# Optimization experiments

Measured on AMD Instinct MI355X. Metric: run time of the kernel, lower is better.

## Reference

```python
import jax, jax.numpy as jnp
import numpy as np
import math

B, C, H, W = 16, 256, 128, 128
N = 4096
D = 256  # out_channels
IMG = 512


def _bilinear_sample(features, grid):
    """features (B,C,H,W), grid (B,N,2) in [-1,1] (x,y). align_corners=True, border padding."""
    Bq, Cq, Hq, Wq = features.shape
    ix = (grid[..., 0] + 1.0) * 0.5 * (Wq - 1)  # (B,N)
    iy = (grid[..., 1] + 1.0) * 0.5 * (Hq - 1)
    # border padding: clamp continuous coords into valid range
    ix = jnp.clip(ix, 0.0, Wq - 1)
    iy = jnp.clip(iy, 0.0, Hq - 1)
    x0 = jnp.floor(ix)
    y0 = jnp.floor(iy)
    wx = ix - x0
    wy = iy - y0
    x0i = jnp.clip(x0.astype(jnp.int32), 0, Wq - 1)
    y0i = jnp.clip(y0.astype(jnp.int32), 0, Hq - 1)
    x1i = jnp.clip(x0i + 1, 0, Wq - 1)
    y1i = jnp.clip(y0i + 1, 0, Hq - 1)
    f = features.reshape(Bq, Cq, Hq * Wq)

    def gather(yi, xi):
        idx = (yi * Wq + xi)[:, None, :]  # (B,1,N)
        return jnp.take_along_axis(f, idx, axis=2)  # (B,C,N)

    v00 = gather(y0i, x0i)
    v01 = gather(y0i, x1i)
    v10 = gather(y1i, x0i)
    v11 = gather(y1i, x1i)
    wx = wx[:, None, :]
    wy = wy[:, None, :]
    top = v00 * (1 - wx) + v01 * wx
    bot = v10 * (1 - wx) + v11 * wx
    return top * (1 - wy) + bot * wy  # (B,C,N)


def _pos_encoding(positions, d_model):
    """positions (B,N,2) in [0,1] -> (B,N,2*d_model) sinusoidal."""
    div_term = jnp.exp(jnp.arange(0, d_model, 2, dtype=jnp.float32)
                       * (-math.log(10000.0) / d_model))  # (d_model//2,)
    x = positions[..., 0:1] * 1000.0  # (B,N,1)
    y = positions[..., 1:2] * 1000.0

    def interleave(v):
        a = v * div_term  # (B,N,d_model//2)
        sc = jnp.stack([jnp.sin(a), jnp.cos(a)], axis=-1)  # (B,N,d//2,2)
        return sc.reshape(*v.shape[:-1], d_model)

    return jnp.concatenate([interleave(x), interleave(y)], axis=-1)


def setup_inputs() -> dict:
    key = jax.random.key(0)
    ks = jax.random.split(key, 8)
    features = jax.random.normal(ks[0], (B, C, H, W), dtype=jnp.float32)
    vertices = jax.random.uniform(ks[1], (B, N, 2), dtype=jnp.float32) * IMG
    s1 = 1.0 / math.sqrt(C)
    s2 = 1.0 / math.sqrt(D)
    W1 = jax.random.uniform(ks[2], (C, D), jnp.float32, -s1, s1)
    b1 = jnp.zeros((D,), jnp.float32)
    W2 = jax.random.uniform(ks[3], (D, D), jnp.float32, -s2, s2)
    b2 = jnp.zeros((D,), jnp.float32)
    Wp = jax.random.uniform(ks[4], (D, D), jnp.float32, -s2, s2)
    bp = jnp.zeros((D,), jnp.float32)
    return {"features": features, "vertices": vertices, "image_size": IMG,
            "W1": W1, "b1": b1, "W2": W2, "b2": b2, "Wp": Wp, "bp": bp}


def reference(features, vertices, image_size, W1, b1, W2, b2, Wp, bp):
    # normalize pixel coords to [-1,1] (align_corners=True convention)
    denom = jnp.float32(image_size - 1)
    grid = 2.0 * vertices / denom - 1.0  # (B,N,2)
    sampled = _bilinear_sample(features, grid)  # (B,C,N)
    sampled = jnp.transpose(sampled, (0, 2, 1))  # (B,N,C)
    h = jax.nn.relu(jnp.einsum('bnc,cd->bnd', sampled, W1) + b1)
    vfeat = jnp.einsum('bnd,de->bne', h, W2) + b2  # (B,N,D)
    pos_enc = _pos_encoding(vertices / jnp.float32(image_size), D // 2)  # (B,N,D)
    out = jnp.einsum('bnd,de->bne', vfeat + pos_enc, Wp) + bp
    return out
```

## Files before the change

### kernel.cpp

```cpp
#include <hip/hip_runtime.h>

#define HW 16384
#define Nn 4096

typedef __bf16 bf16x8 __attribute__((ext_vector_type(8)));
typedef unsigned short us8t __attribute__((ext_vector_type(8)));
typedef float f32x4 __attribute__((ext_vector_type(4)));
typedef float f32x16 __attribute__((ext_vector_type(16)));

__device__ __forceinline__ unsigned short f2bf(float f) {
    unsigned int u = __float_as_uint(f);
    u = (u + 0x7fffu + ((u >> 16) & 1u)) >> 16;
    return (unsigned short)u;
}
__device__ __forceinline__ float bf2f(unsigned int h) {
    return __uint_as_float(h << 16);
}
__device__ __forceinline__ f32x4 mfma16(us8t a, us8t b, f32x4 c) {
    return __builtin_amdgcn_mfma_f32_16x16x32_bf16(
        __builtin_bit_cast(bf16x8, a), __builtin_bit_cast(bf16x8, b), c, 0, 0, 0);
}
__device__ __forceinline__ f32x16 mfma32(us8t a, us8t b, f32x16 c) {
    return __builtin_amdgcn_mfma_f32_32x32x16_bf16(
        __builtin_bit_cast(bf16x8, a), __builtin_bit_cast(bf16x8, b), c, 0, 0, 0);
}

__global__ __launch_bounds__(256) void k_wt(const float* __restrict__ W1,
                                            const float* __restrict__ W2,
                                            const float* __restrict__ Wp,
                                            unsigned short* __restrict__ WT) {
    const int m = blockIdx.x >> 8;
    const int d = blockIdx.x & 255;
    const int c = threadIdx.x;
    const float* W = (m == 0) ? W1 : (m == 1) ? W2 : Wp;
    WT[m * 65536 + d * 256 + c] = f2bf(W[c * 256 + d]);
}

__global__ __launch_bounds__(256) void k_gemm1(const float* __restrict__ f,
                                               const unsigned short* __restrict__ W1T,
                                               unsigned short* __restrict__ S, int b0) {
    __shared__ __align__(16) unsigned short Asb[2][64][32];

    int blk = blockIdx.x;
    if ((gridDim.x & 7) == 0) {
        const int chunk = gridDim.x >> 3;
        blk = (blk & 7) * chunk + (blk >> 3);
    }
    const int bl = blk >> 8;
    const int b = b0 + bl;
    const int p0 = (blk & 255) << 6;
    const int t = threadIdx.x;
    const int lane = t & 63;
    const int w = t >> 6;
    const int l5 = lane >> 5;
    const int r31 = lane & 31;

    const float* fb = f + ((size_t)b << 22) + p0 + lane;

    unsigned short* wP = &Asb[0][lane][(w ^ ((lane >> 2) & 3)) << 3];
    const int G = (r31 >> 2) & 3;
    const unsigned short* rP0 = &Asb[0][r31][(l5 ^ G) << 3];
    const unsigned short* rP1 = &Asb[0][r31][((2 + l5) ^ G) << 3];

    f32x16 acc[2][2];
#pragma unroll
    for (int i = 0; i < 2; ++i)
#pragma unroll
        for (int j = 0; j < 2; ++j)
#pragma unroll
            for (int r = 0; r < 16; ++r) acc[i][j][r] = 0.f;

    const unsigned short* Bp0 = W1T + (((w << 6) + r31) << 8) + (l5 << 3);
    const unsigned short* Bp1 = Bp0 + (32 << 8);

    float pf[8];
#pragma unroll
    for (int j = 0; j < 8; ++j) pf[j] = fb[(size_t)((w << 3) + j) << 14];

    us8t bnx[2][2];
    bnx[0][0] = *(const us8t*)(Bp0);
    bnx[0][1] = *(const us8t*)(Bp0 + 16);
    bnx[1][0] = *(const us8t*)(Bp1);
    bnx[1][1] = *(const us8t*)(Bp1 + 16);

    for (int k0 = 0; k0 < 256; k0 += 32) {
        const int bo = ((k0 >> 5) & 1) << 11;

        uint4 pk;
        pk.x = (unsigned)f2bf(pf[0]) | ((unsigned)f2bf(pf[1]) << 16);
        pk.y = (unsigned)f2bf(pf[2]) | ((unsigned)f2bf(pf[3]) << 16);
        pk.z = (unsigned)f2bf(pf[4]) | ((unsigned)f2bf(pf[5]) << 16);
        pk.w = (unsigned)f2bf(pf[6]) | ((unsigned)f2bf(pf[7]) << 16);
        *(uint4*)(wP + bo) = pk;

        us8t bcur[2][2];
        bcur[0][0] = bnx[0][0]; bcur[0][1] = bnx[0][1];
        bcur[1][0] = bnx[1][0]; bcur[1][1] = bnx[1][1];

        if (k0 < 224) {
#pragma unroll
            for (int j = 0; j < 8; ++j)
                pf[j] = fb[(size_t)(k0 + 32 + (w << 3) + j) << 14];
            bnx[0][0] = *(const us8t*)(Bp0 + k0 + 32);
            bnx[0][1] = *(const us8t*)(Bp0 + k0 + 48);
            bnx[1][0] = *(const us8t*)(Bp1 + k0 + 32);
            bnx[1][1] = *(const us8t*)(Bp1 + k0 + 48);
        }

        __syncthreads();

        us8t af[2][2];
        af[0][0] = *(const us8t*)(rP0 + bo);
        af[0][1] = *(const us8t*)(rP1 + bo);
        af[1][0] = *(const us8t*)(rP0 + bo + 1024);
        af[1][1] = *(const us8t*)(rP1 + bo + 1024);

#pragma unroll
        for (int mt = 0; mt < 2; ++mt)
#pragma unroll
            for (int nt = 0; nt < 2; ++nt) {
                acc[mt][nt] = mfma32(af[mt][0], bcur[nt][0], acc[mt][nt]);
                acc[mt][nt] = mfma32(af[mt][1], bcur[nt][1], acc[mt][nt]);
            }
    }

    unsigned short* Sp = S + ((((size_t)bl << 14) + p0) << 8);
    const int rbase = l5 << 2;
#pragma unroll
    for (int mt = 0; mt < 2; ++mt)
#pragma unroll
        for (int nt = 0; nt < 2; ++nt) {
            const int d = (w << 6) + (nt << 5) + r31;
#pragma unroll
            for (int r = 0; r < 16; ++r) {
                const int row = (mt << 5) + ((r >> 2) << 3) + (r & 3) + rbase;
                Sp[((size_t)row << 8) + d] = f2bf(acc[mt][nt][r]);
            }
        }
}

__global__ __launch_bounds__(256) void k_fused(const unsigned short* __restrict__ S,
                                               const float* __restrict__ verts,
                                               const int* __restrict__ iszp,
                                               const unsigned short* __restrict__ W2T,
                                               const unsigned short* __restrict__ WpT,
                                               const float* __restrict__ b1,
                                               const float* __restrict__ b2,
                                               const float* __restrict__ bpv,
                                               float* __restrict__ out, int b0) {
    __shared__ __align__(16) unsigned short hT[64][264];
    __shared__ __align__(16) int pIdx[64][4];
    __shared__ __align__(16) float wBl[64][4];
    __shared__ float vps[64][2];
    __shared__ __align__(16) float b1s[256];
    __shared__ float b2s[256], bps[256];

    const int blk = blockIdx.x;
    const int bl = blk >> 6;
    const int b = b0 + bl;
    const int n0 = (blk & 63) << 6;
    const int t = threadIdx.x;
    const int lane = t & 63;
    const int w = t >> 6;

    b1s[t] = b1[t];
    b2s[t] = b2[t];
    bps[t] = bpv[t];

    if (t < 64) {
        const float isz = (float)iszp[0];
        const size_t vo = ((size_t)b * Nn + n0 + t) << 1;
        const float vx = verts[vo + 0];
        const float vy = verts[vo + 1];
        const float gs = 127.0f / (isz - 1.0f);
        const float ix = fminf(fmaxf(vx * gs, 0.0f), 127.0f);
        const float iy = fminf(fmaxf(vy * gs, 0.0f), 127.0f);
        const float x0 = floorf(ix), y0 = floorf(iy);
        const float wx = ix - x0, wy = iy - y0;
        const int x0i = (int)x0, y0i = (int)y0;
        const int x1i = min(x0i + 1, 127), y1i = min(y0i + 1, 127);
        pIdx[t][0] = (y0i << 7) + x0i;
        pIdx[t][1] = (y0i << 7) + x1i;
        pIdx[t][2] = (y1i << 7) + x0i;
        pIdx[t][3] = (y1i << 7) + x1i;
        wBl[t][0] = (1.0f - wx) * (1.0f - wy);
        wBl[t][1] = wx * (1.0f - wy);
        wBl[t][2] = (1.0f - wx) * wy;
        wBl[t][3] = wx * wy;
        vps[t][0] = vx / isz;
        vps[t][1] = vy / isz;
    }
    __syncthreads();

    {
        const unsigned short* Sb = S + ((size_t)bl << 22);
        const float4 bl1 = *(const float4*)&b1s[lane << 2];
        for (int i = 0; i < 16; ++i) {
            const int r = (w << 4) + i;
            const int4 pp = *(const int4*)pIdx[r];
            const float4 wt = *(const float4*)wBl[r];
            const uint2 a0 = *(const uint2*)(Sb + ((size_t)pp.x << 8) + (lane << 2));
            const uint2 a1 = *(const uint2*)(Sb + ((size_t)pp.y << 8) + (lane << 2));
            const uint2 a2 = *(const uint2*)(Sb + ((size_t)pp.z << 8) + (lane << 2));
            const uint2 a3 = *(const uint2*)(Sb + ((size_t)pp.w << 8) + (lane << 2));
            float d0 = wt.x * bf2f(a0.x & 0xffffu) + wt.y * bf2f(a1.x & 0xffffu) +
                       wt.z * bf2f(a2.x & 0xffffu) + wt.w * bf2f(a3.x & 0xffffu) + bl1.x;
            float d1 = wt.x * bf2f(a0.x >> 16) + wt.y * bf2f(a1.x >> 16) +
                       wt.z * bf2f(a2.x >> 16) + wt.w * bf2f(a3.x >> 16) + bl1.y;
            float d2 = wt.x * bf2f(a0.y & 0xffffu) + wt.y * bf2f(a1.y & 0xffffu) +
                       wt.z * bf2f(a2.y & 0xffffu) + wt.w * bf2f(a3.y & 0xffffu) + bl1.z;
            float d3 = wt.x * bf2f(a0.y >> 16) + wt.y * bf2f(a1.y >> 16) +
                       wt.z * bf2f(a2.y >> 16) + wt.w * bf2f(a3.y >> 16) + bl1.w;
            d0 = fmaxf(d0, 0.0f);
            d1 = fmaxf(d1, 0.0f);
            d2 = fmaxf(d2, 0.0f);
            d3 = fmaxf(d3, 0.0f);
            uint2 pk;
            pk.x = (unsigned)f2bf(d0) | ((unsigned)f2bf(d1) << 16);
            pk.y = (unsigned)f2bf(d2) | ((unsigned)f2bf(d3) << 16);
            *(uint2*)&hT[r][lane << 2] = pk;
        }
    }
    __syncthreads();

    const int mrow = lane & 15;
    const int kg = (lane >> 4) << 3;
    const int r0 = (lane >> 4) << 2;
    const int n0w = w << 6;

    f32x4 acc[4][4];
#pragma unroll
    for (int i = 0; i < 4; ++i)
#pragma unroll
        for (int j = 0; j < 4; ++j) acc[i][j] = (f32x4){0.f, 0.f, 0.f, 0.f};

    us8t bnx[4];
#pragma unroll
    for (int nt = 0; nt < 4; ++nt)
        bnx[nt] = *(const us8t*)(W2T + ((n0w + (nt << 4) + mrow) << 8) + kg);
    for (int k0 = 0; k0 < 256; k0 += 32) {
        us8t bcur[4];
#pragma unroll
        for (int nt = 0; nt < 4; ++nt) bcur[nt] = bnx[nt];
        if (k0 < 224) {
#pragma unroll
            for (int nt = 0; nt < 4; ++nt)
                bnx[nt] = *(const us8t*)(W2T + ((n0w + (nt << 4) + mrow) << 8) + k0 + 32 + kg);
        }
        us8t af[4];
#pragma unroll
        for (int mt = 0; mt < 4; ++mt)
            af[mt] = *(const us8t*)&hT[(mt << 4) + mrow][k0 + kg];
#pragma unroll
        for (int mt = 0; mt < 4; ++mt)
#pragma unroll
            for (int nt = 0; nt < 4; ++nt)
                acc[mt][nt] = mfma16(af[mt], bcur[nt], acc[mt][nt]);
    }
    __syncthreads();

    const float C2 = -0.20762050593046f;
#pragma unroll
    for (int nt = 0; nt < 4; ++nt) {
        const int col = n0w + (nt << 4) + mrow;
        const float bias2 = b2s[col];
        const int ci = col & 127;
        const float dv = exp2f((float)(ci >> 1) * C2) * 1000.0f;
        const int sel = col >> 7;
#pragma unroll
        for (int mt = 0; mt < 4; ++mt)
#pragma unroll
            for (int j = 0; j < 4; ++j) {
                const int row = (mt << 4) + r0 + j;
                const float ang = vps[row][sel] * dv;
                const float pe = (col & 1) ? __cosf(ang) : __sinf(ang);
                hT[row][col] = f2bf(acc[mt][nt][j] + bias2 + pe);
            }
    }
    __syncthreads();

#pragma unroll
    for (int i = 0; i < 4; ++i)
#pragma unroll
        for (int j = 0; j < 4; ++j) acc[i][j] = (f32x4){0.f, 0.f, 0.f, 0.f};
#pragma unroll
    for (int nt = 0; nt < 4; ++nt)
        bnx[nt] = *(const us8t*)(WpT + ((n0w + (nt << 4) + mrow) << 8) + kg);
    for (int k0 = 0; k0 < 256; k0 += 32) {
        us8t bcur[4];
#pragma unroll
        for (int nt = 0; nt < 4; ++nt) bcur[nt] = bnx[nt];
        if (k0 < 224) {
#pragma unroll
            for (int nt = 0; nt < 4; ++nt)
                bnx[nt] = *(const us8t*)(WpT + ((n0w + (nt << 4) + mrow) << 8) + k0 + 32 + kg);
        }
        us8t af[4];
#pragma unroll
        for (int mt = 0; mt < 4; ++mt)
            af[mt] = *(const us8t*)&hT[(mt << 4) + mrow][k0 + kg];
#pragma unroll
        for (int mt = 0; mt < 4; ++mt)
#pragma unroll
            for (int nt = 0; nt < 4; ++nt)
                acc[mt][nt] = mfma16(af[mt], bcur[nt], acc[mt][nt]);
    }

    float* ob = out + (((size_t)b * Nn + n0) << 8);
#pragma unroll
    for (int nt = 0; nt < 4; ++nt) {
        const int col = n0w + (nt << 4) + mrow;
        const float bb = bps[col];
#pragma unroll
        for (int mt = 0; mt < 4; ++mt)
#pragma unroll
            for (int j = 0; j < 4; ++j) {
                const int row = (mt << 4) + r0 + j;
                ob[((size_t)row << 8) + col] = acc[mt][nt][j] + bb;
            }
    }
}

extern "C" void kernel_launch(void* const* d_in, const int* in_sizes, int n_in,
                              void* d_out, int out_size, void* d_ws, size_t ws_size,
                              hipStream_t stream) {
    const float* f = (const float*)d_in[0];
    const float* verts = (const float*)d_in[1];
    const int* isz = (const int*)d_in[2];
    const float* W1 = (const float*)d_in[3];
    const float* b1 = (const float*)d_in[4];
    const float* W2 = (const float*)d_in[5];
    const float* b2 = (const float*)d_in[6];
    const float* Wp = (const float*)d_in[7];
    const float* bp = (const float*)d_in[8];
    float* out = (float*)d_out;

    unsigned short* WT = (unsigned short*)d_ws;
    const size_t S_OFF = 512u << 10;
    unsigned short* S = (unsigned short*)((char*)d_ws + S_OFF);

    const size_t perBatch = (size_t)HW * 256 * 2;
    size_t sbytes = (ws_size > S_OFF) ? (ws_size - S_OFF) : 0;
    int nbMax = (int)(sbytes / perBatch);
    if (nbMax < 1) nbMax = 1;
    if (nbMax > 16) nbMax = 16;

    k_wt<<<dim3(768), dim3(256), 0, stream>>>(W1, W2, Wp, WT);
    for (int b0 = 0; b0 < 16; b0 += nbMax) {
        const int nb = (16 - b0 < nbMax) ? (16 - b0) : nbMax;
        k_gemm1<<<dim3(nb * 256), dim3(256), 0, stream>>>(f, WT, S, b0);
        k_fused<<<dim3(nb * 64), dim3(256), 0, stream>>>(S, verts, isz, WT + 65536, WT + 131072,
                                                         b1, b2, bp, out, b0);
    }
}
```

Measured before the change: 525.4 us.

## Restructure first GEMM with larger tiles and async global-to-LDS fp32 staging

The feature-projection GEMM is rebuilt around 512-thread blocks, each covering 256 pixels by all 256 output channels instead of 64 pixels. Feature tiles of 64 channels are copied as fp32 straight from global memory into double-buffered shared memory with the global_load_lds builtin, and converted to bf16 when read for MFMA. W1T fragments are now loaded from global memory inside the inner loop instead of being prefetched into registers. The aim is to cut register round-trips and grid count, and to overlap the feature stream with compute. The cost is 128 KB of LDS per block, which limits residency to one block per CU despite the launch bound of two, plus repeated conversions on every LDS read.

```diff
diff --git a/kernel.cpp b/kernel.cpp
--- a/kernel.cpp
+++ b/kernel.cpp
@@ -23,6 +23,12 @@
 __device__ __forceinline__ f32x16 mfma32(us8t a, us8t b, f32x16 c) {
     return __builtin_amdgcn_mfma_f32_32x32x16_bf16(
         __builtin_bit_cast(bf16x8, a), __builtin_bit_cast(bf16x8, b), c, 0, 0, 0);
+}
+
+__device__ __forceinline__ void gload16(const float* g, float* l) {
+    __builtin_amdgcn_global_load_lds(
+        (const __attribute__((address_space(1))) unsigned int*)g,
+        (__attribute__((address_space(3))) unsigned int*)l, 16, 0, 0);
 }
 
 __global__ __launch_bounds__(256) void k_wt(const float* __restrict__ W1,
@@ -36,92 +42,76 @@
     WT[m * 65536 + d * 256 + c] = f2bf(W[c * 256 + d]);
 }
 
-__global__ __launch_bounds__(256) void k_gemm1(const float* __restrict__ f,
-                                               const unsigned short* __restrict__ W1T,
-                                               unsigned short* __restrict__ S, int b0) {
-    __shared__ __align__(16) unsigned short Asb[2][64][32];
+__global__ __launch_bounds__(512, 2) void k_gemm1(const float* __restrict__ f,
+                                                  const unsigned short* __restrict__ W1T,
+                                                  unsigned short* __restrict__ S, int b0) {
+    __shared__ __align__(16) float fs[2][64][256];
 
     int blk = blockIdx.x;
     if ((gridDim.x & 7) == 0) {
         const int chunk = gridDim.x >> 3;
         blk = (blk & 7) * chunk + (blk >> 3);
     }
-    const int bl = blk >> 8;
+    const int bl = blk >> 6;
     const int b = b0 + bl;
-    const int p0 = (blk & 255) << 6;
+    const int p0 = (blk & 63) << 8;
     const int t = threadIdx.x;
     const int lane = t & 63;
     const int w = t >> 6;
     const int l5 = lane >> 5;
     const int r31 = lane & 31;
-
-    const float* fb = f + ((size_t)b << 22) + p0 + lane;
-
-    unsigned short* wP = &Asb[0][lane][(w ^ ((lane >> 2) & 3)) << 3];
-    const int G = (r31 >> 2) & 3;
-    const unsigned short* rP0 = &Asb[0][r31][(l5 ^ G) << 3];
-    const unsigned short* rP1 = &Asb[0][r31][((2 + l5) ^ G) << 3];
-
-    f32x16 acc[2][2];
+    const int wp = w & 3;
+    const int wd = w >> 2;
+
+    const float* fb = f + ((size_t)b << 22) + p0;
+
+    f32x16 acc[2][4];
 #pragma unroll
     for (int i = 0; i < 2; ++i)
 #pragma unroll
-        for (int j = 0; j < 2; ++j)
+        for (int j = 0; j < 4; ++j)
 #pragma unroll
             for (int r = 0; r < 16; ++r) acc[i][j][r] = 0.f;
 
-    const unsigned short* Bp0 = W1T + (((w << 6) + r31) << 8) + (l5 << 3);
-    const unsigned short* Bp1 = Bp0 + (32 << 8);
-
-    float pf[8];
-#pragma unroll
-    for (int j = 0; j < 8; ++j) pf[j] = fb[(size_t)((w << 3) + j) << 14];
-
-    us8t bnx[2][2];
-    bnx[0][0] = *(const us8t*)(Bp0);
-    bnx[0][1] = *(const us8t*)(Bp0 + 16);
-    bnx[1][0] = *(const us8t*)(Bp1);
-    bnx[1][1] = *(const us8t*)(Bp1 + 16);
-
-    for (int k0 = 0; k0 < 256; k0 += 32) {
-        const int bo = ((k0 >> 5) & 1) << 11;
-
-        uint4 pk;
-        pk.x = (unsigned)f2bf(pf[0]) | ((unsigned)f2bf(pf[1]) << 16);
-        pk.y = (unsigned)f2bf(pf[2]) | ((unsigned)f2bf(pf[3]) << 16);
-        pk.z = (unsigned)f2bf(pf[4]) | ((unsigned)f2bf(pf[5]) << 16);
-        pk.w = (unsigned)f2bf(pf[6]) | ((unsigned)f2bf(pf[7]) << 16);
-        *(uint4*)(wP + bo) = pk;
-
-        us8t bcur[2][2];
-        bcur[0][0] = bnx[0][0]; bcur[0][1] = bnx[0][1];
-        bcur[1][0] = bnx[1][0]; bcur[1][1] = bnx[1][1];
-
-        if (k0 < 224) {
-#pragma unroll
-            for (int j = 0; j < 8; ++j)
-                pf[j] = fb[(size_t)(k0 + 32 + (w << 3) + j) << 14];
-            bnx[0][0] = *(const us8t*)(Bp0 + k0 + 32);
-            bnx[0][1] = *(const us8t*)(Bp0 + k0 + 48);
-            bnx[1][0] = *(const us8t*)(Bp1 + k0 + 32);
-            bnx[1][1] = *(const us8t*)(Bp1 + k0 + 48);
-        }
-
+    auto stage = [&](int bufi, int kt) {
+#pragma unroll
+        for (int i = 0; i < 8; ++i) {
+            const int c = (w << 3) + i;
+            gload16(fb + ((size_t)(((kt) << 6) + c) << 14) + (lane << 2), &fs[bufi][c][0]);
+        }
+    };
+
+    stage(0, 0);
+    __syncthreads();
+
+    const int plA = (wp << 6) + r31;
+
+    for (int kt = 0; kt < 4; ++kt) {
+        const int cur = kt & 1;
+        if (kt < 3) stage(cur ^ 1, kt + 1);
+
+#pragma unroll
+        for (int h = 0; h < 4; ++h) {
+            const int cb = (h << 4) + (l5 << 3);
+            us8t A[2];
+#pragma unroll
+            for (int mt = 0; mt < 2; ++mt) {
+                const int pl = plA + (mt << 5);
+                float av[8];
+#pragma unroll
+                for (int j = 0; j < 8; ++j) av[j] = fs[cur][cb + j][pl];
+#pragma unroll
+                for (int j = 0; j < 8; ++j) A[mt][j] = f2bf(av[j]);
+            }
+#pragma unroll
+            for (int nt = 0; nt < 4; ++nt) {
+                const int col = (wd << 7) + (nt << 5) + r31;
+                const us8t bfr = *(const us8t*)(W1T + (col << 8) + (kt << 6) + cb);
+                acc[0][nt] = mfma32(A[0], bfr, acc[0][nt]);
+                acc[1][nt] = mfma32(A[1], bfr, acc[1][nt]);
+            }
+        }
         __syncthreads();
-
-        us8t af[2][2];
-        af[0][0] = *(const us8t*)(rP0 + bo);
-        af[0][1] = *(const us8t*)(rP1 + bo);
-        af[1][0] = *(const us8t*)(rP0 + bo + 1024);
-        af[1][1] = *(const us8t*)(rP1 + bo + 1024);
-
-#pragma unroll
-        for (int mt = 0; mt < 2; ++mt)
-#pragma unroll
-            for (int nt = 0; nt < 2; ++nt) {
-                acc[mt][nt] = mfma32(af[mt][0], bcur[nt][0], acc[mt][nt]);
-                acc[mt][nt] = mfma32(af[mt][1], bcur[nt][1], acc[mt][nt]);
-            }
     }
 
     unsigned short* Sp = S + ((((size_t)bl << 14) + p0) << 8);
@@ -129,11 +119,11 @@
 #pragma unroll
     for (int mt = 0; mt < 2; ++mt)
 #pragma unroll
-        for (int nt = 0; nt < 2; ++nt) {
-            const int d = (w << 6) + (nt << 5) + r31;
+        for (int nt = 0; nt < 4; ++nt) {
+            const int d = (wd << 7) + (nt << 5) + r31;
 #pragma unroll
             for (int r = 0; r < 16; ++r) {
-                const int row = (mt << 5) + ((r >> 2) << 3) + (r & 3) + rbase;
+                const int row = (wp << 6) + (mt << 5) + ((r >> 2) << 3) + (r & 3) + rbase;
                 Sp[((size_t)row << 8) + d] = f2bf(acc[mt][nt][r]);
             }
         }
@@ -348,7 +338,7 @@
     k_wt<<<dim3(768), dim3(256), 0, stream>>>(W1, W2, Wp, WT);
     for (int b0 = 0; b0 < 16; b0 += nbMax) {
         const int nb = (16 - b0 < nbMax) ? (16 - b0) : nbMax;
-        k_gemm1<<<dim3(nb * 256), dim3(256), 0, stream>>>(f, WT, S, b0);
+        k_gemm1<<<dim3(nb * 64), dim3(512), 0, stream>>>(f, WT, S, b0);
         k_fused<<<dim3(nb * 64), dim3(256), 0, stream>>>(S, verts, isz, WT + 65536, WT + 131072,
                                                          b1, b2, bp, out, b0);
     }
```

Result: no change. 520.6 us (-0.9%).
